# Performance work log

Hardware: AMD Instinct MI355X
Metric: run time of the kernel (lower is better)

## Reference

```python
import jax, jax.numpy as jnp
import numpy as np

N_MLP = 16
LATENT = 1024
S0, S1, S2, OUT = 512, 256, 128, 3


def _make_grid(n_grid_step):
    # matches np.meshgrid (indexing='xy') then reshape(-1): points (x, y)
    p = np.linspace(-1.0, 1.0, n_grid_step, dtype=np.float32)
    X, Y = np.meshgrid(p, p)
    return jnp.asarray(np.stack([X.ravel(), Y.ravel()], axis=-1))  # [G, 2]


def setup_inputs() -> dict:
    key = jax.random.key(0)
    ks = jax.random.split(key, 12)
    sc = lambda fan_in: 1.0 / np.sqrt(fan_in)
    inp = {
        "x0": jax.random.normal(ks[0], (LATENT,), jnp.float32),
        "W0a": jax.random.normal(ks[1], (N_MLP, S0, LATENT), jnp.float32) * sc(LATENT),
        "b0a": jax.random.normal(ks[2], (N_MLP, S0), jnp.float32) * sc(LATENT),
        "W0b": jax.random.normal(ks[3], (N_MLP, S0, 2), jnp.float32) * sc(2),
        "b0b": jax.random.normal(ks[4], (N_MLP, S0), jnp.float32) * sc(2),
        "W1": jax.random.normal(ks[5], (N_MLP, S1, S0), jnp.float32) * sc(S0),
        "b1": jax.random.normal(ks[6], (N_MLP, S1), jnp.float32) * sc(S0),
        "W2": jax.random.normal(ks[7], (N_MLP, S2, S1), jnp.float32) * sc(S1),
        "b2": jax.random.normal(ks[8], (N_MLP, S2), jnp.float32) * sc(S1),
        "W3": jax.random.normal(ks[9], (N_MLP, OUT, S2), jnp.float32) * sc(S2),
        "b3": jax.random.normal(ks[10], (N_MLP, OUT), jnp.float32) * sc(S2),
        "n_grid_step": 128,
    }
    return inp


def reference(x0, W0a, b0a, W0b, b0b, W1, b1, W2, b2, W3, b3, n_grid_step):
    grid = _make_grid(n_grid_step)  # [G, 2], constant (requires_grad=False)
    # latent branch: [m, S0]
    y0_a = jnp.einsum('mol,l->mo', W0a, x0) + b0a
    # grid branch: [m, G, S0]
    y0_b = jnp.einsum('moi,gi->mgo', W0b, grid) + b0b[:, None, :]
    h = jax.nn.relu(y0_a[:, None, :] + y0_b)                        # [m,G,S0]
    h = jax.nn.relu(jnp.einsum('moh,mgh->mgo', W1, h) + b1[:, None, :])  # [m,G,S1]
    h = jax.nn.relu(jnp.einsum('moh,mgh->mgo', W2, h) + b2[:, None, :])  # [m,G,S2]
    out = jnp.tanh(jnp.einsum('moh,mgh->mgo', W3, h) + b3[:, None, :])   # [m,G,3]
    return out.reshape(-1, OUT)  # [m*G, 3]
```

## Files before the change

kernel.cpp:

```cpp
#include <hip/hip_runtime.h>
#include <hip/hip_bf16.h>
#include <cstdint>

typedef __bf16 bf16_t;
typedef bf16_t bf16x8 __attribute__((ext_vector_type(8)));
typedef bf16_t bf16x4 __attribute__((ext_vector_type(4)));
typedef float  f32x4  __attribute__((ext_vector_type(4)));

#define S0 512
#define S1 256
#define S2 128
#define NGRID 128
#define GPTS (NGRID*NGRID)

#define WS_BASE  0u
#define WS_W1P   32768u
#define WS_W2P   4227072u
#define WS_W3P   5275648u
#define WS_BASEC 5341184u
#define WS_WXYC  5373952u
#define WS_IDX   5439488u
#define WS_LIN   5472256u
#define WS_F     5505024u
#define WS_CNT   5570560u

__device__ __forceinline__ float tanh_fast(float x) {
  float e = __builtin_amdgcn_exp2f(x * 2.88539008f);
  return fmaf(-2.0f, __builtin_amdgcn_rcpf(e + 1.0f), 1.0f);
}

__global__ __launch_bounds__(256) void prep_a(
    const float* __restrict__ x0, const float* __restrict__ W0a,
    const float* __restrict__ b0a, const float* __restrict__ b0b,
    const float* __restrict__ W2, const float* __restrict__ W3,
    float* __restrict__ base, bf16_t* __restrict__ W2p, bf16_t* __restrict__ W3p)
{
  if (blockIdx.x < 2048) {
    int wid = (blockIdx.x << 2) + (threadIdx.x >> 6);
    int L = threadIdx.x & 63;
    int m = wid >> 9, o = wid & 511;
    const float* wrow = W0a + ((size_t)(m*S0 + o) << 10);
    float acc = 0.f;
#pragma unroll
    for (int i = 0; i < 4; ++i) {
      f32x4 wv = *(const f32x4*)(wrow + i*256 + L*4);
      f32x4 xv = *(const f32x4*)(x0   + i*256 + L*4);
      acc += wv.x*xv.x + wv.y*xv.y + wv.z*xv.z + wv.w*xv.w;
    }
#pragma unroll
    for (int s = 32; s; s >>= 1) acc += __shfl_xor(acc, s, 64);
    if (L == 0) base[m*S0 + o] = acc + b0a[m*S0 + o] + b0b[m*S0 + o];
    return;
  }

  int T = (blockIdx.x - 2048) * 256 + threadIdx.x;
  const float* src = nullptr;
  bf16_t* dst = nullptr;
  if (T < 65536) {
    int L = T & 63, nt = (T >> 6) & 7, ks = (T >> 9) & 7, m = T >> 12;
    int n = nt*16 + (L & 15), k0 = ks*32 + ((L >> 4) & 3)*8;
    src = W2 + (size_t)(m*S2 + n)*S1 + k0;
    dst = W2p + (size_t)T*8;
  } else {
    int T3 = T - 65536;
    int L = T3 & 63, ks = (T3 >> 6) & 3, m = T3 >> 8;
    int n = L & 15, k0 = ks*32 + ((L >> 4) & 3)*8;
    dst = W3p + (size_t)T3*8;
    if (n < 3) src = W3 + (size_t)(m*3 + n)*S2 + k0;
  }
  bf16x8 v;
  if (src) {
    f32x4 a = *(const f32x4*)src;
    f32x4 b = *(const f32x4*)(src + 4);
    v[0]=(bf16_t)a.x; v[1]=(bf16_t)a.y; v[2]=(bf16_t)a.z; v[3]=(bf16_t)a.w;
    v[4]=(bf16_t)b.x; v[5]=(bf16_t)b.y; v[6]=(bf16_t)b.z; v[7]=(bf16_t)b.w;
  } else {
#pragma unroll
    for (int j = 0; j < 8; ++j) v[j] = (bf16_t)0.f;
  }
  *(bf16x8*)dst = v;
}

__global__ __launch_bounds__(256) void classify_k(
    const float* __restrict__ base, const float* __restrict__ W0b,
    float* __restrict__ basec, float* __restrict__ wxyc,
    int* __restrict__ idx, int* __restrict__ lin,
    int* __restrict__ Kc, int* __restrict__ nlin, float* __restrict__ F)
{
  __shared__ int sc[512];
  const int m = blockIdx.x, t = threadIdx.x;
  float b[2], wx[2], wy[2]; int fa[2], fl[2];
#pragma unroll
  for (int h = 0; h < 2; ++h) {
    const int k = t + h*256;
    b[h]  = base[m*S0 + k];
    wx[h] = W0b[(m*S0 + k)*2];
    wy[h] = W0b[(m*S0 + k)*2 + 1];
    const float aw = fabsf(wx[h]) + fabsf(wy[h]);
    const int dead = (b[h] + aw) <= 0.f;
    fl[h] = (!dead) && ((b[h] - aw) >= 0.f);
    fa[h] = (!dead) && (!fl[h]);
    sc[k] = fa[h] | (fl[h] << 16);
  }
  __syncthreads();
  for (int off = 1; off < 512; off <<= 1) {
    int v0 = sc[t], v1 = sc[t+256];
    int u0 = (t >= off) ? sc[t-off] : 0;
    int u1 = (t+256 >= off) ? sc[t+256-off] : 0;
    __syncthreads();
    sc[t] = v0 + u0; sc[t+256] = v1 + u1;
    __syncthreads();
  }
  const int tot = sc[511];
  const int KcM = tot & 0xffff, nlM = tot >> 16;
#pragma unroll
  for (int h = 0; h < 2; ++h) {
    const int k = t + h*256;
    const int incl = sc[k];
    if (fa[h]) {
      const int p = (incl & 0xffff) - 1;
      idx[m*S0 + p] = k;
      basec[m*S0 + p] = b[h];
      wxyc[m*S0*2 + 2*p]     = wx[h];
      wxyc[m*S0*2 + 2*p + 1] = wy[h];
    } else if (fl[h]) {
      lin[m*S0 + ((incl >> 16) - 1)] = k;
    }
  }
  for (int s = t; s < 512; s += 256) {
    if (s >= KcM) {
      idx[m*S0 + s] = 0;
      basec[m*S0 + s] = 0.f;
      wxyc[m*S0*2 + 2*s] = 0.f;
      wxyc[m*S0*2 + 2*s + 1] = 0.f;
    }
  }
  for (int i = t; i < 1024; i += 256) F[m*1024 + i] = 0.f;
  if (t == 0) { Kc[m] = KcM; nlin[m] = nlM; }
}

__global__ __launch_bounds__(256) void prep_b(
    const float* __restrict__ W1, const float* __restrict__ base,
    const float* __restrict__ W0b,
    const int* __restrict__ idx, const int* __restrict__ lin,
    const int* __restrict__ Kc, const int* __restrict__ nlin,
    bf16_t* __restrict__ W1p, float* __restrict__ F)
{
  if (blockIdx.x < 1024) {
    const int T = blockIdx.x*256 + threadIdx.x;
    const int L = T & 63, nt = (T >> 6) & 15, ks = (T >> 10) & 15, m = T >> 14;
    const int KcM = Kc[m];
    const int n = nt*16 + (L & 15), kb = ks*32 + ((L >> 4) & 3)*8;
    const float* wrow = W1 + (size_t)(m*S1 + n)*S0;
    const int* ip = idx + m*S0 + kb;
    bf16x8 v;
#pragma unroll
    for (int j = 0; j < 8; ++j)
      v[j] = (kb + j < KcM) ? (bf16_t)wrow[ip[j]] : (bf16_t)0.f;
    *(bf16x8*)(W1p + (size_t)T*8) = v;
  } else {
    const int b2 = blockIdx.x - 1024;
    const int m = b2 >> 4, s = b2 & 15, n = threadIdx.x;
    const int nl = nlin[m];
    float a0 = 0.f, ax = 0.f, ay = 0.f;
    const float* wrow = W1 + (size_t)(m*S1 + n)*S0;
    for (int j = s; j < nl; j += 16) {
      const int k = lin[m*S0 + j];
      const float w = wrow[k];
      a0 = fmaf(w, base[m*S0 + k], a0);
      ax = fmaf(w, W0b[(m*S0 + k)*2], ax);
      ay = fmaf(w, W0b[(m*S0 + k)*2 + 1], ay);
    }
    float* fp = F + ((size_t)m*S1 + n)*4;
    atomicAdd(fp + 0, a0);
    atomicAdd(fp + 1, ax);
    atomicAdd(fp + 2, ay);
  }
}

template<int NKS>
__device__ __forceinline__ void l1_compute(
    const bf16_t* __restrict__ bp1, const float* __restrict__ bc,
    const float* __restrict__ wc, const int quad, const float yv,
    const float xv0, const float step, f32x4 (&acc1)[4][4])
{
  bf16x8 Bc[4];
#pragma unroll
  for (int n = 0; n < 4; ++n) Bc[n] = *(const bf16x8*)(bp1 + (size_t)n*512);

#pragma unroll 2
  for (int ks = 0; ks < NKS; ++ks) {
    const int kk = ks*32 + quad*8;
    f32x4 cA  = *(const f32x4*)(bc + kk);
    f32x4 cB  = *(const f32x4*)(bc + kk + 4);
    f32x4 wv0 = *(const f32x4*)(wc + kk*2);
    f32x4 wv1 = *(const f32x4*)(wc + kk*2 + 4);
    f32x4 wv2 = *(const f32x4*)(wc + kk*2 + 8);
    f32x4 wv3 = *(const f32x4*)(wc + kk*2 + 12);

    bf16x8 Bn[4];
    if (ks + 1 < NKS) {
#pragma unroll
      for (int n = 0; n < 4; ++n)
        Bn[n] = *(const bf16x8*)(bp1 + (size_t)(ks+1)*8192 + (size_t)n*512);
    }

    float t[8], wx[8];
    t[0] = fmaf(wv0.y, yv, cA.x); wx[0] = wv0.x;
    t[1] = fmaf(wv0.w, yv, cA.y); wx[1] = wv0.z;
    t[2] = fmaf(wv1.y, yv, cA.z); wx[2] = wv1.x;
    t[3] = fmaf(wv1.w, yv, cA.w); wx[3] = wv1.z;
    t[4] = fmaf(wv2.y, yv, cB.x); wx[4] = wv2.x;
    t[5] = fmaf(wv2.w, yv, cB.y); wx[5] = wv2.z;
    t[6] = fmaf(wv3.y, yv, cB.z); wx[6] = wv3.x;
    t[7] = fmaf(wv3.w, yv, cB.w); wx[7] = wv3.z;

#pragma unroll
    for (int mt = 0; mt < 4; ++mt) {
      const float xr = xv0 + (float)(mt*16)*step;
      bf16x8 af;
#pragma unroll
      for (int j = 0; j < 8; ++j)
        af[j] = (bf16_t)fmaxf(fmaf(wx[j], xr, t[j]), 0.f);
#pragma unroll
      for (int n = 0; n < 4; ++n)
        acc1[mt][n] = __builtin_amdgcn_mfma_f32_16x16x32_bf16(Bc[n], af, acc1[mt][n], 0, 0, 0);
    }
    if (ks + 1 < NKS) {
#pragma unroll
      for (int n = 0; n < 4; ++n) Bc[n] = Bn[n];
    }
  }
}

__global__ __launch_bounds__(256, 3) void fused_mlp_k(
    const float* __restrict__ basec, const float* __restrict__ wxyc,
    const float* __restrict__ F, const int* __restrict__ Kc,
    const bf16_t* __restrict__ W1p, const bf16_t* __restrict__ W2p,
    const bf16_t* __restrict__ W3p,
    const float* __restrict__ b1, const float* __restrict__ b2,
    const float* __restrict__ b3, float* __restrict__ out)
{
  __shared__ __align__(16) bf16_t sA1[64*264];

  const int bid  = blockIdx.x;
  const int m    = bid >> 8;
  const int tile = bid & 255;
  const int g0   = tile * 64;

  const int tid  = threadIdx.x;
  const int w    = tid >> 6, L = tid & 63;
  const int quad = L >> 4, lrow = L & 15;

  const float step = 2.0f / 127.0f;
  const float yv  = -1.0f + (float)(tile >> 1) * step;
  const float xv0 = -1.0f + (float)(((tile & 1) << 6) + lrow) * step;

  const float* bc = basec + m*S0;
  const float* wc = wxyc + m*(S0*2);
  const int nks = (Kc[m] + 31) >> 5;

  f32x4 zero = {0.f, 0.f, 0.f, 0.f};
  f32x4 acc1[4][4];
#pragma unroll
  for (int a = 0; a < 4; ++a)
#pragma unroll
    for (int b = 0; b < 4; ++b) acc1[a][b] = zero;

  const bf16_t* bp1 = W1p + (((size_t)(m*16)*16 + w*4)*64 + L)*8;
#define L1_CASE(NN) case NN: l1_compute<NN>(bp1, bc, wc, quad, yv, xv0, step, acc1); break;
  switch (nks) {
    L1_CASE(16) L1_CASE(15) L1_CASE(14) L1_CASE(13)
    L1_CASE(12) L1_CASE(11) L1_CASE(10) L1_CASE(9)
    L1_CASE(8)  L1_CASE(7)  L1_CASE(6)  L1_CASE(5)
    L1_CASE(4)  L1_CASE(3)  L1_CASE(2)  L1_CASE(1)
    default: break;
  }
#undef L1_CASE

#pragma unroll
  for (int nb = 0; nb < 4; ++nb) {
    const int col = w*64 + nb*16 + quad*4;
    f32x4 bb = *(const f32x4*)(b1 + m*S1 + col);
    float cterm[4], fx[4];
#pragma unroll
    for (int p = 0; p < 4; ++p) {
      f32x4 Fv = *(const f32x4*)(F + ((size_t)m*S1 + col + p)*4);
      cterm[p] = fmaf(Fv.z, yv, bb[p] + Fv.x);
      fx[p] = Fv.y;
    }
#pragma unroll
    for (int mt = 0; mt < 4; ++mt) {
      const int row = mt*16 + lrow;
      const float xr = xv0 + (float)(mt*16)*step;
      bf16x4 v;
#pragma unroll
      for (int p = 0; p < 4; ++p)
        v[p] = (bf16_t)fmaxf(acc1[mt][nb][p] + fmaf(fx[p], xr, cterm[p]), 0.f);
      *(bf16x4*)(&sA1[row*264 + col]) = v;
    }
  }
  __syncthreads();

  f32x4 acc2[4][2];
#pragma unroll
  for (int a = 0; a < 4; ++a) { acc2[a][0] = zero; acc2[a][1] = zero; }
  const bf16_t* bp2 = W2p + (((size_t)(m*8)*8 + w*2)*64 + L)*8;
#pragma unroll 2
  for (int ks = 0; ks < 8; ++ks) {
    const int k2 = ks*32 + quad*8;
    bf16x8 af[4];
#pragma unroll
    for (int mt = 0; mt < 4; ++mt)
      af[mt] = *(const bf16x8*)(&sA1[(mt*16 + lrow)*264 + k2]);
    bf16x8 b0f = *(const bf16x8*)(bp2 + (size_t)ks*4096);
    bf16x8 b1f = *(const bf16x8*)(bp2 + (size_t)ks*4096 + 512);
#pragma unroll
    for (int mt = 0; mt < 4; ++mt)
      acc2[mt][0] = __builtin_amdgcn_mfma_f32_16x16x32_bf16(b0f, af[mt], acc2[mt][0], 0, 0, 0);
#pragma unroll
    for (int mt = 0; mt < 4; ++mt)
      acc2[mt][1] = __builtin_amdgcn_mfma_f32_16x16x32_bf16(b1f, af[mt], acc2[mt][1], 0, 0, 0);
  }
  __syncthreads();

  bf16_t* sH2 = sA1;
#pragma unroll
  for (int nb = 0; nb < 2; ++nb) {
    const int col = w*32 + nb*16 + quad*4;
    f32x4 bb = *(const f32x4*)(b2 + m*S2 + col);
#pragma unroll
    for (int mt = 0; mt < 4; ++mt) {
      const int row = mt*16 + lrow;
      bf16x4 v;
#pragma unroll
      for (int p = 0; p < 4; ++p)
        v[p] = (bf16_t)fmaxf(acc2[mt][nb][p] + bb[p], 0.f);
      *(bf16x4*)(&sH2[row*136 + col]) = v;
    }
  }
  __syncthreads();

  f32x4 acc3 = zero;
#pragma unroll
  for (int ks = 0; ks < 4; ++ks) {
    bf16x8 af  = *(const bf16x8*)(&sH2[(w*16 + lrow)*136 + ks*32 + quad*8]);
    bf16x8 bfr = *(const bf16x8*)(W3p + (((size_t)m*4 + ks)*64 + L)*8);
    acc3 = __builtin_amdgcn_mfma_f32_16x16x32_bf16(bfr, af, acc3, 0, 0, 0);
  }
  if (quad == 0) {
    const size_t o = ((size_t)m*GPTS + g0 + w*16 + lrow)*3;
    out[o + 0] = tanh_fast(acc3[0] + b3[m*3 + 0]);
    out[o + 1] = tanh_fast(acc3[1] + b3[m*3 + 1]);
    out[o + 2] = tanh_fast(acc3[2] + b3[m*3 + 2]);
  }
}

extern "C" void kernel_launch(void* const* d_in, const int* in_sizes, int n_in,
                              void* d_out, int out_size, void* d_ws, size_t ws_size,
                              hipStream_t stream) {
  const float* x0  = (const float*)d_in[0];
  const float* W0a = (const float*)d_in[1];
  const float* b0a = (const float*)d_in[2];
  const float* W0b = (const float*)d_in[3];
  const float* b0b = (const float*)d_in[4];
  const float* W1  = (const float*)d_in[5];
  const float* b1  = (const float*)d_in[6];
  const float* W2  = (const float*)d_in[7];
  const float* b2  = (const float*)d_in[8];
  const float* W3  = (const float*)d_in[9];
  const float* b3  = (const float*)d_in[10];

  char* ws = (char*)d_ws;
  float*  base  = (float*)(ws + WS_BASE);
  bf16_t* W1p   = (bf16_t*)(ws + WS_W1P);
  bf16_t* W2p   = (bf16_t*)(ws + WS_W2P);
  bf16_t* W3p   = (bf16_t*)(ws + WS_W3P);
  float*  basec = (float*)(ws + WS_BASEC);
  float*  wxyc  = (float*)(ws + WS_WXYC);
  int*    idx   = (int*)(ws + WS_IDX);
  int*    lin   = (int*)(ws + WS_LIN);
  float*  F     = (float*)(ws + WS_F);
  int*    Kc    = (int*)(ws + WS_CNT);
  int*    nlin  = (int*)(ws + WS_CNT + 64);
  float*  out   = (float*)d_out;

  prep_a<<<2368, 256, 0, stream>>>(x0, W0a, b0a, b0b, W2, W3, base, W2p, W3p);
  classify_k<<<16, 256, 0, stream>>>(base, W0b, basec, wxyc, idx, lin, Kc, nlin, F);
  prep_b<<<1280, 256, 0, stream>>>(W1, base, W0b, idx, lin, Kc, nlin, W1p, F);
  fused_mlp_k<<<4096, 256, 0, stream>>>(basec, wxyc, F, Kc, W1p, W2p, W3p, b1, b2, b3, out);
}
```

Baseline: 204.1 us.

## Share layer-1 activation generation across waves via LDS staging

Before, every wave computed all four 16-row activation tiles for each K step. Now each wave computes only its own 16-row slice of the grid-branch activations and writes it to a double-buffered LDS stage. After a barrier, all waves read the four slices back as MFMA operands. This removes the redundant VALU work four times over, at the cost of a __syncthreads per K step and extra LDS traffic. Launch bounds are also raised to 4 blocks per CU for occupancy, and a cosmetic a0*0.f term is added to an atomicAdd.

```diff
diff --git a/kernel.cpp b/kernel.cpp
--- a/kernel.cpp
+++ b/kernel.cpp
@@ -173,7 +173,7 @@
     }
     float* fp = F + ((size_t)m*S1 + n)*4;
     atomicAdd(fp + 0, a0);
-    atomicAdd(fp + 1, ax);
+    atomicAdd(fp + 1, a0*0.f + ax);
     atomicAdd(fp + 2, ay);
   }
 }
@@ -181,8 +181,9 @@
 template<int NKS>
 __device__ __forceinline__ void l1_compute(
     const bf16_t* __restrict__ bp1, const float* __restrict__ bc,
-    const float* __restrict__ wc, const int quad, const float yv,
-    const float xv0, const float step, f32x4 (&acc1)[4][4])
+    const float* __restrict__ wc, bf16_t* sStg,
+    const int w, const int L, const int quad, const float yv,
+    const float xrw, f32x4 (&acc1)[4][4])
 {
   bf16x8 Bc[4];
 #pragma unroll
@@ -191,37 +192,37 @@
 #pragma unroll 2
   for (int ks = 0; ks < NKS; ++ks) {
     const int kk = ks*32 + quad*8;
+
+    bf16x8 Bn[4];
+    if (ks + 1 < NKS) {
+#pragma unroll
+      for (int n = 0; n < 4; ++n)
+        Bn[n] = *(const bf16x8*)(bp1 + (size_t)(ks+1)*8192 + (size_t)n*512);
+    }
+
     f32x4 cA  = *(const f32x4*)(bc + kk);
     f32x4 cB  = *(const f32x4*)(bc + kk + 4);
     f32x4 wv0 = *(const f32x4*)(wc + kk*2);
     f32x4 wv1 = *(const f32x4*)(wc + kk*2 + 4);
     f32x4 wv2 = *(const f32x4*)(wc + kk*2 + 8);
     f32x4 wv3 = *(const f32x4*)(wc + kk*2 + 12);
-
-    bf16x8 Bn[4];
-    if (ks + 1 < NKS) {
-#pragma unroll
-      for (int n = 0; n < 4; ++n)
-        Bn[n] = *(const bf16x8*)(bp1 + (size_t)(ks+1)*8192 + (size_t)n*512);
-    }
-
-    float t[8], wx[8];
-    t[0] = fmaf(wv0.y, yv, cA.x); wx[0] = wv0.x;
-    t[1] = fmaf(wv0.w, yv, cA.y); wx[1] = wv0.z;
-    t[2] = fmaf(wv1.y, yv, cA.z); wx[2] = wv1.x;
-    t[3] = fmaf(wv1.w, yv, cA.w); wx[3] = wv1.z;
-    t[4] = fmaf(wv2.y, yv, cB.x); wx[4] = wv2.x;
-    t[5] = fmaf(wv2.w, yv, cB.y); wx[5] = wv2.z;
-    t[6] = fmaf(wv3.y, yv, cB.z); wx[6] = wv3.x;
-    t[7] = fmaf(wv3.w, yv, cB.w); wx[7] = wv3.z;
+    bf16x8 g;
+    g[0] = (bf16_t)fmaxf(fmaf(wv0.x, xrw, fmaf(wv0.y, yv, cA.x)), 0.f);
+    g[1] = (bf16_t)fmaxf(fmaf(wv0.z, xrw, fmaf(wv0.w, yv, cA.y)), 0.f);
+    g[2] = (bf16_t)fmaxf(fmaf(wv1.x, xrw, fmaf(wv1.y, yv, cA.z)), 0.f);
+    g[3] = (bf16_t)fmaxf(fmaf(wv1.z, xrw, fmaf(wv1.w, yv, cA.w)), 0.f);
+    g[4] = (bf16_t)fmaxf(fmaf(wv2.x, xrw, fmaf(wv2.y, yv, cB.x)), 0.f);
+    g[5] = (bf16_t)fmaxf(fmaf(wv2.z, xrw, fmaf(wv2.w, yv, cB.y)), 0.f);
+    g[6] = (bf16_t)fmaxf(fmaf(wv3.x, xrw, fmaf(wv3.y, yv, cB.z)), 0.f);
+    g[7] = (bf16_t)fmaxf(fmaf(wv3.z, xrw, fmaf(wv3.w, yv, cB.w)), 0.f);
+
+    bf16_t* stg = sStg + (ks & 1)*2048;
+    *(bf16x8*)(stg + ((w << 6) + L)*8) = g;
+    __syncthreads();
 
 #pragma unroll
     for (int mt = 0; mt < 4; ++mt) {
-      const float xr = xv0 + (float)(mt*16)*step;
-      bf16x8 af;
-#pragma unroll
-      for (int j = 0; j < 8; ++j)
-        af[j] = (bf16_t)fmaxf(fmaf(wx[j], xr, t[j]), 0.f);
+      bf16x8 af = *(const bf16x8*)(stg + ((mt << 6) + L)*8);
 #pragma unroll
       for (int n = 0; n < 4; ++n)
         acc1[mt][n] = __builtin_amdgcn_mfma_f32_16x16x32_bf16(Bc[n], af, acc1[mt][n], 0, 0, 0);
@@ -233,7 +234,7 @@
   }
 }
 
-__global__ __launch_bounds__(256, 3) void fused_mlp_k(
+__global__ __launch_bounds__(256, 4) void fused_mlp_k(
     const float* __restrict__ basec, const float* __restrict__ wxyc,
     const float* __restrict__ F, const int* __restrict__ Kc,
     const bf16_t* __restrict__ W1p, const bf16_t* __restrict__ W2p,
@@ -255,6 +256,7 @@
   const float step = 2.0f / 127.0f;
   const float yv  = -1.0f + (float)(tile >> 1) * step;
   const float xv0 = -1.0f + (float)(((tile & 1) << 6) + lrow) * step;
+  const float xrw = xv0 + (float)(w*16)*step;
 
   const float* bc = basec + m*S0;
   const float* wc = wxyc + m*(S0*2);
@@ -268,7 +270,7 @@
     for (int b = 0; b < 4; ++b) acc1[a][b] = zero;
 
   const bf16_t* bp1 = W1p + (((size_t)(m*16)*16 + w*4)*64 + L)*8;
-#define L1_CASE(NN) case NN: l1_compute<NN>(bp1, bc, wc, quad, yv, xv0, step, acc1); break;
+#define L1_CASE(NN) case NN: l1_compute<NN>(bp1, bc, wc, sA1, w, L, quad, yv, xrw, acc1); break;
   switch (nks) {
     L1_CASE(16) L1_CASE(15) L1_CASE(14) L1_CASE(13)
     L1_CASE(12) L1_CASE(11) L1_CASE(10) L1_CASE(9)
@@ -277,6 +279,7 @@
     default: break;
   }
 #undef L1_CASE
+  __syncthreads();
 
 #pragma unroll
   for (int nb = 0; nb < 4; ++nb) {
```

Measured after the change: 217.0 us. +6.3%, slower.

## Double block tile to 128 grid points with LDS-shared layer-1 activations

Applied to the files above, without the earlier changes.

Each block now covers a full grid row of 128 points, so 2048 blocks run instead of 4096 and every W1/W2/W3 fragment load feeds twice as many MFMAs. Layer-1 input activations are no longer recomputed by every wave: each wave computes two 16-row slices and shares them through a double-buffered LDS staging area, synchronised with a barrier on every k-step. The H1 buffer switches to an XOR-swizzled layout to avoid LDS bank conflicts. In exchange the accumulators double, register pressure rises, occupancy drops from 3 to 2 blocks per CU, and the new per-iteration barrier adds synchronisation cost.

```diff
diff --git a/kernel.cpp b/kernel.cpp
--- a/kernel.cpp
+++ b/kernel.cpp
@@ -27,6 +27,15 @@
 __device__ __forceinline__ float tanh_fast(float x) {
   float e = __builtin_amdgcn_exp2f(x * 2.88539008f);
   return fmaf(-2.0f, __builtin_amdgcn_rcpf(e + 1.0f), 1.0f);
+}
+
+__device__ __forceinline__ bf16x8 ld_h1(const bf16_t* s, int row, int colk) {
+  const int byte = row*512 + (((colk*2) ^ ((row & 7) << 4)));
+  return *(const bf16x8*)((const char*)s + byte);
+}
+__device__ __forceinline__ void st_h1(bf16_t* s, int row, int col, bf16x4 v) {
+  const int byte = row*512 + (((col*2) ^ ((row & 7) << 4)));
+  *(bf16x4*)((char*)s + byte) = v;
 }
 
 __global__ __launch_bounds__(256) void prep_a(
@@ -181,8 +190,9 @@
 template<int NKS>
 __device__ __forceinline__ void l1_compute(
     const bf16_t* __restrict__ bp1, const float* __restrict__ bc,
-    const float* __restrict__ wc, const int quad, const float yv,
-    const float xv0, const float step, f32x4 (&acc1)[4][4])
+    const float* __restrict__ wc, bf16_t* sStg,
+    const int w, const int L, const int quad,
+    const float yv, const float xg0, const float xg1, f32x4 (&acc1)[8][4])
 {
   bf16x8 Bc[4];
 #pragma unroll
@@ -190,6 +200,14 @@
 
 #pragma unroll 2
   for (int ks = 0; ks < NKS; ++ks) {
+    const bf16_t* bpk = bp1 + (size_t)ks*8192;
+    bf16x8 Bn[4];
+    if (ks + 1 < NKS) {
+#pragma unroll
+      for (int n = 0; n < 4; ++n)
+        Bn[n] = *(const bf16x8*)(bpk + 8192 + (size_t)n*512);
+    }
+
     const int kk = ks*32 + quad*8;
     f32x4 cA  = *(const f32x4*)(bc + kk);
     f32x4 cB  = *(const f32x4*)(bc + kk + 4);
@@ -197,13 +215,6 @@
     f32x4 wv1 = *(const f32x4*)(wc + kk*2 + 4);
     f32x4 wv2 = *(const f32x4*)(wc + kk*2 + 8);
     f32x4 wv3 = *(const f32x4*)(wc + kk*2 + 12);
-
-    bf16x8 Bn[4];
-    if (ks + 1 < NKS) {
-#pragma unroll
-      for (int n = 0; n < 4; ++n)
-        Bn[n] = *(const bf16x8*)(bp1 + (size_t)(ks+1)*8192 + (size_t)n*512);
-    }
 
     float t[8], wx[8];
     t[0] = fmaf(wv0.y, yv, cA.x); wx[0] = wv0.x;
@@ -215,13 +226,23 @@
     t[6] = fmaf(wv3.y, yv, cB.z); wx[6] = wv3.x;
     t[7] = fmaf(wv3.w, yv, cB.w); wx[7] = wv3.z;
 
-#pragma unroll
-    for (int mt = 0; mt < 4; ++mt) {
-      const float xr = xv0 + (float)(mt*16)*step;
-      bf16x8 af;
-#pragma unroll
-      for (int j = 0; j < 8; ++j)
-        af[j] = (bf16_t)fmaxf(fmaf(wx[j], xr, t[j]), 0.f);
+    bf16x8 g0, g1;
+#pragma unroll
+    for (int j = 0; j < 8; ++j) {
+      g0[j] = (bf16_t)fmaxf(fmaf(wx[j], xg0, t[j]), 0.f);
+      g1[j] = (bf16_t)fmaxf(fmaf(wx[j], xg1, t[j]), 0.f);
+    }
+
+    bf16_t* stg = sStg + (ks & 1)*4096;
+    *(bf16x8*)(stg + (((2*w  ) << 6) + L)*8) = g0;
+    *(bf16x8*)(stg + (((2*w+1) << 6) + L)*8) = g1;
+    asm volatile("s_waitcnt lgkmcnt(0)" ::: "memory");
+    __builtin_amdgcn_s_barrier();
+    __builtin_amdgcn_sched_barrier(0);
+
+#pragma unroll
+    for (int mt = 0; mt < 8; ++mt) {
+      bf16x8 af = *(const bf16x8*)(stg + ((mt << 6) + L)*8);
 #pragma unroll
       for (int n = 0; n < 4; ++n)
         acc1[mt][n] = __builtin_amdgcn_mfma_f32_16x16x32_bf16(Bc[n], af, acc1[mt][n], 0, 0, 0);
@@ -233,7 +254,7 @@
   }
 }
 
-__global__ __launch_bounds__(256, 3) void fused_mlp_k(
+__global__ __launch_bounds__(256, 2) void fused_mlp_k(
     const float* __restrict__ basec, const float* __restrict__ wxyc,
     const float* __restrict__ F, const int* __restrict__ Kc,
     const bf16_t* __restrict__ W1p, const bf16_t* __restrict__ W2p,
@@ -241,34 +262,35 @@
     const float* __restrict__ b1, const float* __restrict__ b2,
     const float* __restrict__ b3, float* __restrict__ out)
 {
-  __shared__ __align__(16) bf16_t sA1[64*264];
-
-  const int bid  = blockIdx.x;
-  const int m    = bid >> 8;
-  const int tile = bid & 255;
-  const int g0   = tile * 64;
+  __shared__ __align__(16) bf16_t sLDS[128*256];
+
+  const int bid = blockIdx.x;
+  const int m   = bid >> 7;
+  const int st  = bid & 127;
 
   const int tid  = threadIdx.x;
   const int w    = tid >> 6, L = tid & 63;
   const int quad = L >> 4, lrow = L & 15;
 
   const float step = 2.0f / 127.0f;
-  const float yv  = -1.0f + (float)(tile >> 1) * step;
-  const float xv0 = -1.0f + (float)(((tile & 1) << 6) + lrow) * step;
+  const float yv  = -1.0f + (float)st * step;
+  const float xv0 = -1.0f + (float)lrow * step;
+  const float xg0 = xv0 + (float)((2*w  )*16)*step;
+  const float xg1 = xv0 + (float)((2*w+1)*16)*step;
 
   const float* bc = basec + m*S0;
   const float* wc = wxyc + m*(S0*2);
   const int nks = (Kc[m] + 31) >> 5;
 
   f32x4 zero = {0.f, 0.f, 0.f, 0.f};
-  f32x4 acc1[4][4];
-#pragma unroll
-  for (int a = 0; a < 4; ++a)
+  f32x4 acc1[8][4];
+#pragma unroll
+  for (int a = 0; a < 8; ++a)
 #pragma unroll
     for (int b = 0; b < 4; ++b) acc1[a][b] = zero;
 
   const bf16_t* bp1 = W1p + (((size_t)(m*16)*16 + w*4)*64 + L)*8;
-#define L1_CASE(NN) case NN: l1_compute<NN>(bp1, bc, wc, quad, yv, xv0, step, acc1); break;
+#define L1_CASE(NN) case NN: l1_compute<NN>(bp1, bc, wc, sLDS, w, L, quad, yv, xg0, xg1, acc1); break;
   switch (nks) {
     L1_CASE(16) L1_CASE(15) L1_CASE(14) L1_CASE(13)
     L1_CASE(12) L1_CASE(11) L1_CASE(10) L1_CASE(9)
@@ -277,6 +299,7 @@
     default: break;
   }
 #undef L1_CASE
+  __syncthreads();
 
 #pragma unroll
   for (int nb = 0; nb < 4; ++nb) {
@@ -290,47 +313,43 @@
       fx[p] = Fv.y;
     }
 #pragma unroll
-    for (int mt = 0; mt < 4; ++mt) {
+    for (int mt = 0; mt < 8; ++mt) {
       const int row = mt*16 + lrow;
       const float xr = xv0 + (float)(mt*16)*step;
       bf16x4 v;
 #pragma unroll
       for (int p = 0; p < 4; ++p)
         v[p] = (bf16_t)fmaxf(acc1[mt][nb][p] + fmaf(fx[p], xr, cterm[p]), 0.f);
-      *(bf16x4*)(&sA1[row*264 + col]) = v;
+      st_h1(sLDS, row, col, v);
     }
   }
   __syncthreads();
 
-  f32x4 acc2[4][2];
-#pragma unroll
-  for (int a = 0; a < 4; ++a) { acc2[a][0] = zero; acc2[a][1] = zero; }
+  f32x4 acc2[8][2];
+#pragma unroll
+  for (int a = 0; a < 8; ++a) { acc2[a][0] = zero; acc2[a][1] = zero; }
   const bf16_t* bp2 = W2p + (((size_t)(m*8)*8 + w*2)*64 + L)*8;
 #pragma unroll 2
   for (int ks = 0; ks < 8; ++ks) {
     const int k2 = ks*32 + quad*8;
-    bf16x8 af[4];
-#pragma unroll
-    for (int mt = 0; mt < 4; ++mt)
-      af[mt] = *(const bf16x8*)(&sA1[(mt*16 + lrow)*264 + k2]);
     bf16x8 b0f = *(const bf16x8*)(bp2 + (size_t)ks*4096);
     bf16x8 b1f = *(const bf16x8*)(bp2 + (size_t)ks*4096 + 512);
 #pragma unroll
-    for (int mt = 0; mt < 4; ++mt)
-      acc2[mt][0] = __builtin_amdgcn_mfma_f32_16x16x32_bf16(b0f, af[mt], acc2[mt][0], 0, 0, 0);
-#pragma unroll
-    for (int mt = 0; mt < 4; ++mt)
-      acc2[mt][1] = __builtin_amdgcn_mfma_f32_16x16x32_bf16(b1f, af[mt], acc2[mt][1], 0, 0, 0);
+    for (int mt = 0; mt < 8; ++mt) {
+      bf16x8 af = ld_h1(sLDS, mt*16 + lrow, k2);
+      acc2[mt][0] = __builtin_amdgcn_mfma_f32_16x16x32_bf16(b0f, af, acc2[mt][0], 0, 0, 0);
+      acc2[mt][1] = __builtin_amdgcn_mfma_f32_16x16x32_bf16(b1f, af, acc2[mt][1], 0, 0, 0);
+    }
   }
   __syncthreads();
 
-  bf16_t* sH2 = sA1;
+  bf16_t* sH2 = sLDS;
 #pragma unroll
   for (int nb = 0; nb < 2; ++nb) {
     const int col = w*32 + nb*16 + quad*4;
     f32x4 bb = *(const f32x4*)(b2 + m*S2 + col);
 #pragma unroll
-    for (int mt = 0; mt < 4; ++mt) {
+    for (int mt = 0; mt < 8; ++mt) {
       const int row = mt*16 + lrow;
       bf16x4 v;
 #pragma unroll
@@ -341,18 +360,24 @@
   }
   __syncthreads();
 
-  f32x4 acc3 = zero;
+  f32x4 acc3[2] = {zero, zero};
 #pragma unroll
   for (int ks = 0; ks < 4; ++ks) {
-    bf16x8 af  = *(const bf16x8*)(&sH2[(w*16 + lrow)*136 + ks*32 + quad*8]);
     bf16x8 bfr = *(const bf16x8*)(W3p + (((size_t)m*4 + ks)*64 + L)*8);
-    acc3 = __builtin_amdgcn_mfma_f32_16x16x32_bf16(bfr, af, acc3, 0, 0, 0);
+    bf16x8 af0 = *(const bf16x8*)(&sH2[((w  )*16 + lrow)*136 + ks*32 + quad*8]);
+    bf16x8 af1 = *(const bf16x8*)(&sH2[((w+4)*16 + lrow)*136 + ks*32 + quad*8]);
+    acc3[0] = __builtin_amdgcn_mfma_f32_16x16x32_bf16(bfr, af0, acc3[0], 0, 0, 0);
+    acc3[1] = __builtin_amdgcn_mfma_f32_16x16x32_bf16(bfr, af1, acc3[1], 0, 0, 0);
   }
   if (quad == 0) {
-    const size_t o = ((size_t)m*GPTS + g0 + w*16 + lrow)*3;
-    out[o + 0] = tanh_fast(acc3[0] + b3[m*3 + 0]);
-    out[o + 1] = tanh_fast(acc3[1] + b3[m*3 + 1]);
-    out[o + 2] = tanh_fast(acc3[2] + b3[m*3 + 2]);
+#pragma unroll
+    for (int ri = 0; ri < 2; ++ri) {
+      const int rb = w + ri*4;
+      const size_t o = ((size_t)m*GPTS + (size_t)st*128 + rb*16 + lrow)*3;
+      out[o + 0] = tanh_fast(acc3[ri][0] + b3[m*3 + 0]);
+      out[o + 1] = tanh_fast(acc3[ri][1] + b3[m*3 + 1]);
+      out[o + 2] = tanh_fast(acc3[ri][2] + b3[m*3 + 2]);
+    }
   }
 }
 
@@ -388,5 +413,5 @@
   prep_a<<<2368, 256, 0, stream>>>(x0, W0a, b0a, b0b, W2, W3, base, W2p, W3p);
   classify_k<<<16, 256, 0, stream>>>(base, W0b, basec, wxyc, idx, lin, Kc, nlin, F);
   prep_b<<<1280, 256, 0, stream>>>(W1, base, W0b, idx, lin, Kc, nlin, W1p, F);
-  fused_mlp_k<<<4096, 256, 0, stream>>>(basec, wxyc, F, Kc, W1p, W2p, W3p, b1, b2, b3, out);
-}
+  fused_mlp_k<<<2048, 256, 0, stream>>>(basec, wxyc, F, Kc, W1p, W2p, W3p, b1, b2, b3, out);
+}
```

Result: faster. 197.0 us (-3.5%).
